# Kernel tuning notes

Hardware: AMD Instinct MI355X
Metric: run time of the kernel (lower is better)

## Reference

```python
import jax, jax.numpy as jnp
import numpy as np

D = 256
K = 3  # depthwise conv kernel size (odd)
A_EPS = 1e-4
POW_MIN = 1e-20
LN_EPS = 1e-5


def setup_inputs() -> dict:
    key = jax.random.key(0)
    ks = jax.random.split(key, 10)
    B, H, W = 8, 96, 96
    x = jax.random.normal(ks[0], (B, H, W, D), dtype=jnp.float32)
    inp = {
        'x': x,
        'ln_g': jnp.ones((D,), jnp.float32),
        'ln_b': jnp.zeros((D,), jnp.float32),
        'w_in': jax.random.normal(ks[1], (D, 2 * D), jnp.float32) * 0.02,
        'b_in': jnp.zeros((2 * D,), jnp.float32),
        'conv_w': jax.random.normal(ks[2], (K, K, 1, D), jnp.float32) * 0.1,
        'conv_b': jnp.zeros((D,), jnp.float32),
        'a_logit': 7.0 + 0.1 * jax.random.normal(ks[3], (D,), jnp.float32),
        'ssm_b': jnp.ones((D,), jnp.float32) + 0.02 * jax.random.normal(ks[4], (D,), jnp.float32),
        'ssm_c': jnp.ones((D,), jnp.float32) + 0.02 * jax.random.normal(ks[5], (D,), jnp.float32),
        'ssm_d': jnp.ones((D,), jnp.float32) + 0.02 * jax.random.normal(ks[6], (D,), jnp.float32),
        'w_out': jax.random.normal(ks[7], (D, D), jnp.float32) * 0.02,
        'b_out': jnp.zeros((D,), jnp.float32),
    }
    return inp


def _ssm_scan(x, a_logit, b, c, d):
    # x: (N, L, D). s_t = a*s_{t-1} + b*x_t ; y_t = c*s_t + d*x_t
    # via log-domain cumsum reformulation (as in the torch source).
    L = x.shape[1]
    a = jnp.clip(jax.nn.sigmoid(a_logit), A_EPS, 1.0 - A_EPS)  # (D,)
    t = jnp.arange(L, dtype=jnp.float32)
    a_pow = jnp.maximum(jnp.exp(t[:, None] * jnp.log(a)[None, :]), POW_MIN)  # (L,D)
    u = x * b  # (N,L,D)
    r = jnp.cumsum(u / a_pow[None], axis=1)
    return r * a_pow[None] * c + x * d


def reference(x, ln_g, ln_b, w_in, b_in, conv_w, conv_b,
              a_logit, ssm_b, ssm_c, ssm_d, w_out, b_out):
    B, H, W, Dm = x.shape
    x0 = x
    # LayerNorm over channel dim
    mu = jnp.mean(x, axis=-1, keepdims=True)
    var = jnp.mean(jnp.square(x - mu), axis=-1, keepdims=True)
    h = (x - mu) * jax.lax.rsqrt(var + LN_EPS) * ln_g + ln_b
    # in_proj -> split into value and gate
    xg = h @ w_in + b_in  # (B,H,W,2D)
    x_in, gate = jnp.split(xg, 2, axis=-1)
    gate = jax.nn.sigmoid(gate)
    # depthwise conv (SAME padding) + SiLU, NHWC layout
    u = jax.lax.conv_general_dilated(
        x_in, conv_w, window_strides=(1, 1), padding='SAME',
        dimension_numbers=('NHWC', 'HWIO', 'NHWC'), feature_group_count=Dm)
    u = jax.nn.silu(u + conv_b)
    # 2D bidirectional scan mixing
    L = H * W
    seq_row = u.reshape(B, L, Dm)
    seq_col = u.transpose(0, 2, 1, 3).reshape(B, L, Dm)

    def bid(s):
        yf = _ssm_scan(s, a_logit, ssm_b, ssm_c, ssm_d)
        yb = jnp.flip(_ssm_scan(jnp.flip(s, axis=1), a_logit, ssm_b, ssm_c, ssm_d), axis=1)
        return 0.5 * (yf + yb)

    y_row = bid(seq_row).reshape(B, H, W, Dm)
    y_col = bid(seq_col).reshape(B, W, H, Dm).transpose(0, 2, 1, 3)
    y = 0.5 * (y_row + y_col)
    # gate, out_proj, residual
    y = y * gate
    y = y @ w_out + b_out
    return x0 + y
```

## Files before the change

### kernel.cpp

```cpp
#include <hip/hip_runtime.h>
#include <math.h>

#define DD   256
#define HHH  96
#define WWW  96
#define NB   8
#define LL   9216
#define NPIX (NB*LL)
#define TCH  32
#define NCH  (LL/TCH)

typedef __bf16 bf16_8 __attribute__((ext_vector_type(8)));
typedef float  f32_4  __attribute__((ext_vector_type(4)));

static __device__ __forceinline__ float sigmoidf_(float x) {
    return 1.0f / (1.0f + expf(-x));
}

template<int DIR>
static __device__ __forceinline__ int spidx(int t) {
    if (DIR == 0) return t;
    int w = t / HHH;
    int h = t - w * HHH;
    return h * WWW + w;
}

__global__ __launch_bounds__(256) void wcvt_kernel(const float* __restrict__ w_in,
                                                   const float* __restrict__ w_out,
                                                   __bf16* __restrict__ w_inT,
                                                   __bf16* __restrict__ w_outT) {
    int i = blockIdx.x * 256 + threadIdx.x;
    int n = i >> 8, k = i & 255;
    w_inT[i] = (__bf16)w_in[k * 512 + n];
    if (i < 256 * 256) w_outT[i] = (__bf16)w_out[k * 256 + n];
}

__global__ __launch_bounds__(256) void ln_kernel(const float* __restrict__ x,
                                                 const float* __restrict__ g,
                                                 const float* __restrict__ b,
                                                 __bf16* __restrict__ h) {
    int pix = blockIdx.x;
    int d = threadIdx.x;
    float v = x[(size_t)pix * DD + d];
    float s = v, s2 = v * v;
    #pragma unroll
    for (int o = 32; o > 0; o >>= 1) {
        s  += __shfl_down(s, o, 64);
        s2 += __shfl_down(s2, o, 64);
    }
    __shared__ float ws1[4], ws2[4];
    int wid = d >> 6, lane = d & 63;
    if (lane == 0) { ws1[wid] = s; ws2[wid] = s2; }
    __syncthreads();
    if (d == 0) {
        float a = 0.f, c = 0.f;
        for (int i = 0; i < 4; i++) { a += ws1[i]; c += ws2[i]; }
        ws1[0] = a; ws2[0] = c;
    }
    __syncthreads();
    float mu  = ws1[0] * (1.0f / 256.0f);
    float var = ws2[0] * (1.0f / 256.0f) - mu * mu;
    float r = rsqrtf(var + 1e-5f);
    h[(size_t)pix * DD + d] = (__bf16)((v - mu) * r * g[d] + b[d]);
}

template<int MODE>
__global__ __launch_bounds__(256) void gemm_bf16(const __bf16* __restrict__ A,
                                                 const __bf16* __restrict__ BT,
                                                 const float* __restrict__ bias,
                                                 __bf16* __restrict__ out_xin,
                                                 __bf16* __restrict__ out_gate,
                                                 float* __restrict__ out_f32,
                                                 const float* __restrict__ x0) {
    const int K = 256;
    __shared__ __bf16 As[128 * 40];
    __shared__ __bf16 Bs[128 * 40];
    int tid = threadIdx.x;
    int lane = tid & 63, wv = tid >> 6;
    int rowBase = blockIdx.x * 128;
    int colBase = blockIdx.y * 128;
    int ldr = tid >> 2;
    int seg = tid & 3;

    f32_4 acc[4][4];
    #pragma unroll
    for (int i = 0; i < 4; i++)
        #pragma unroll
        for (int j = 0; j < 4; j++) acc[i][j] = (f32_4){0.f, 0.f, 0.f, 0.f};

    const __bf16* Aip = A + (size_t)(rowBase + ldr) * K + seg * 8;
    const __bf16* Bip = BT + (size_t)(colBase + ldr) * K + seg * 8;
    int m0 = (wv >> 1) * 64, n0 = (wv & 1) * 64;
    int fr = lane & 15, fq = lane >> 4;

    for (int k0 = 0; k0 < K; k0 += 32) {
        uint4 a0 = *(const uint4*)(Aip + k0);
        uint4 a1 = *(const uint4*)(Aip + (size_t)64 * K + k0);
        uint4 b0 = *(const uint4*)(Bip + k0);
        uint4 b1 = *(const uint4*)(Bip + (size_t)64 * K + k0);
        __syncthreads();
        *(uint4*)&As[ldr * 40 + seg * 8]        = a0;
        *(uint4*)&As[(ldr + 64) * 40 + seg * 8] = a1;
        *(uint4*)&Bs[ldr * 40 + seg * 8]        = b0;
        *(uint4*)&Bs[(ldr + 64) * 40 + seg * 8] = b1;
        __syncthreads();
        bf16_8 af[4], bb[4];
        #pragma unroll
        for (int mi = 0; mi < 4; mi++)
            af[mi] = *(const bf16_8*)&As[(m0 + mi * 16 + fr) * 40 + fq * 8];
        #pragma unroll
        for (int ni = 0; ni < 4; ni++)
            bb[ni] = *(const bf16_8*)&Bs[(n0 + ni * 16 + fr) * 40 + fq * 8];
        #pragma unroll
        for (int mi = 0; mi < 4; mi++)
            #pragma unroll
            for (int ni = 0; ni < 4; ni++)
                acc[mi][ni] = __builtin_amdgcn_mfma_f32_16x16x32_bf16(
                    af[mi], bb[ni], acc[mi][ni], 0, 0, 0);
    }

    int rowW = rowBase + m0 + fq * 4;
    int colW = colBase + n0 + fr;
    #pragma unroll
    for (int mi = 0; mi < 4; mi++) {
        #pragma unroll
        for (int ni = 0; ni < 4; ni++) {
            int col = colW + ni * 16;
            float bv = bias[col];
            #pragma unroll
            for (int r = 0; r < 4; r++) {
                int row = rowW + mi * 16 + r;
                float v = acc[mi][ni][r] + bv;
                if (MODE == 0) {
                    if (col < 256) {
                        out_xin[(size_t)row * 256 + col] = (__bf16)v;
                    } else {
                        out_gate[(size_t)row * 256 + (col - 256)] = (__bf16)sigmoidf_(v);
                    }
                } else {
                    out_f32[(size_t)row * 256 + col] = v + x0[(size_t)row * 256 + col];
                }
            }
        }
    }
}

static __device__ __forceinline__ void loadcol(const __bf16* __restrict__ xin,
                                               int b, int h, int w, int d,
                                               float c[3]) {
    if (w < 0 || w >= WWW) { c[0] = c[1] = c[2] = 0.f; return; }
    size_t base = ((size_t)b * LL + (size_t)h * WWW + w) * DD + d;
    c[0] = (h > 0)       ? (float)xin[base - (size_t)WWW * DD] : 0.f;
    c[1] = (float)xin[base];
    c[2] = (h + 1 < HHH) ? (float)xin[base + (size_t)WWW * DD] : 0.f;
}

__global__ __launch_bounds__(256) void conv_tot_kernel(const __bf16* __restrict__ xin,
                                                       const float* __restrict__ cw,
                                                       const float* __restrict__ cb,
                                                       const float* __restrict__ a_logit,
                                                       const float* __restrict__ ssm_b,
                                                       __bf16* __restrict__ u,
                                                       float* __restrict__ tot_f,
                                                       float* __restrict__ tot_b) {
    int cx = blockIdx.x, h = blockIdx.y, b = blockIdx.z;
    int d = threadIdx.x;
    int w0 = cx * TCH;
    float k[9];
    #pragma unroll
    for (int i = 0; i < 9; i++) k[i] = cw[i * DD + d];
    float bias = cb[d];
    float a = sigmoidf_(a_logit[d]);
    a = fminf(fmaxf(a, 1e-4f), 1.0f - 1e-4f);
    float bb = ssm_b[d];

    float cl[3], cc[3], cr[3];
    loadcol(xin, b, h, w0 - 1, d, cl);
    loadcol(xin, b, h, w0,     d, cc);
    loadcol(xin, b, h, w0 + 1, d, cr);

    float v[TCH];
    float sf = 0.f;
    size_t outBase = ((size_t)b * LL + (size_t)h * WWW + w0) * DD + d;
    #pragma unroll
    for (int j = 0; j < TCH; j++) {
        float nx[3];
        loadcol(xin, b, h, w0 + j + 2, d, nx);
        float acc = bias;
        acc += k[0] * cl[0] + k[1] * cc[0] + k[2] * cr[0];
        acc += k[3] * cl[1] + k[4] * cc[1] + k[5] * cr[1];
        acc += k[6] * cl[2] + k[7] * cc[2] + k[8] * cr[2];
        float uv = acc * sigmoidf_(acc);
        v[j] = uv;
        u[outBase + (size_t)j * DD] = (__bf16)uv;
        sf = a * sf + bb * uv;
        cl[0] = cc[0]; cl[1] = cc[1]; cl[2] = cc[2];
        cc[0] = cr[0]; cc[1] = cr[1]; cc[2] = cr[2];
        cr[0] = nx[0]; cr[1] = nx[1]; cr[2] = nx[2];
    }
    int chunk = h * 3 + cx;
    tot_f[((size_t)b * NCH + chunk) * DD + d] = sf;
    float sb = 0.f;
    #pragma unroll
    for (int j = TCH - 1; j >= 0; j--) sb = a * sb + bb * v[j];
    tot_b[((size_t)b * NCH + chunk) * DD + d] = sb;
}

__global__ __launch_bounds__(256) void scan_totals_col(const __bf16* __restrict__ u,
                                                       const float* __restrict__ a_logit,
                                                       const float* __restrict__ ssm_b,
                                                       float* __restrict__ tot_f,
                                                       float* __restrict__ tot_b) {
    int blk = blockIdx.x;
    int b = blk / NCH, c = blk - b * NCH;
    int d = threadIdx.x;
    float a = sigmoidf_(a_logit[d]);
    a = fminf(fmaxf(a, 1e-4f), 1.0f - 1e-4f);
    float bb = ssm_b[d];
    size_t base = (size_t)b * LL * DD;
    int t0 = c * TCH;
    float v[TCH];
    #pragma unroll
    for (int j = 0; j < TCH; j++)
        v[j] = (float)u[base + (size_t)spidx<1>(t0 + j) * DD + d];
    float s = 0.f;
    #pragma unroll
    for (int j = 0; j < TCH; j++) s = a * s + bb * v[j];
    tot_f[(size_t)blk * DD + d] = s;
    s = 0.f;
    #pragma unroll
    for (int j = TCH - 1; j >= 0; j--) s = a * s + bb * v[j];
    tot_b[(size_t)blk * DD + d] = s;
}

__global__ __launch_bounds__(256) void scan_carries(const float* __restrict__ tot_all,
                                                    const float* __restrict__ a_logit,
                                                    float* __restrict__ car_all) {
    int b = blockIdx.x;
    int var = blockIdx.y;
    int d = threadIdx.x;
    float a = sigmoidf_(a_logit[d]);
    a = fminf(fmaxf(a, 1e-4f), 1.0f - 1e-4f);
    float a2 = a * a, a4 = a2 * a2, a8 = a4 * a4, a16 = a8 * a8;
    float q = a16 * a16;
    const float* tot = tot_all + (size_t)var * NB * NCH * DD + (size_t)b * NCH * DD + d;
    float* car = car_all + (size_t)var * NB * NCH * DD + (size_t)b * NCH * DD + d;
    float P = 0.f;
    if ((var & 1) == 0) {
        for (int c0 = 0; c0 < NCH; c0 += 8) {
            float t[8];
            #pragma unroll
            for (int j = 0; j < 8; j++) t[j] = tot[(size_t)(c0 + j) * DD];
            #pragma unroll
            for (int j = 0; j < 8; j++) {
                car[(size_t)(c0 + j) * DD] = P;
                P = q * P + t[j];
            }
        }
    } else {
        for (int c0 = NCH - 8; c0 >= 0; c0 -= 8) {
            float t[8];
            #pragma unroll
            for (int j = 0; j < 8; j++) t[j] = tot[(size_t)(c0 + j) * DD];
            #pragma unroll
            for (int j = 7; j >= 0; j--) {
                car[(size_t)(c0 + j) * DD] = P;
                P = q * P + t[j];
            }
        }
    }
}

template<int DIR>
__global__ __launch_bounds__(256) void scan_apply(const __bf16* __restrict__ u,
                                                  const float* __restrict__ a_logit,
                                                  const float* __restrict__ ssm_b,
                                                  const float* __restrict__ ssm_c,
                                                  const float* __restrict__ ssm_d,
                                                  const float* __restrict__ car_f,
                                                  const float* __restrict__ car_b,
                                                  float* __restrict__ y,
                                                  const __bf16* __restrict__ gate,
                                                  __bf16* __restrict__ g) {
    int blk = blockIdx.x;
    int b = blk / NCH, c = blk - b * NCH;
    int d = threadIdx.x;
    float a = sigmoidf_(a_logit[d]);
    a = fminf(fmaxf(a, 1e-4f), 1.0f - 1e-4f);
    float bb = ssm_b[d], cc = ssm_c[d], dd = ssm_d[d];
    size_t base = (size_t)b * LL * DD;
    int t0 = c * TCH;
    float v[TCH];
    #pragma unroll
    for (int j = 0; j < TCH; j++)
        v[j] = (float)u[base + (size_t)spidx<DIR>(t0 + j) * DD + d];
    float yf[TCH];
    float s = car_f[(size_t)blk * DD + d];
    #pragma unroll
    for (int j = 0; j < TCH; j++) {
        s = a * s + bb * v[j];
        yf[j] = cc * s + dd * v[j];
    }
    s = car_b[(size_t)blk * DD + d];
    #pragma unroll
    for (int j = TCH - 1; j >= 0; j--) {
        s = a * s + bb * v[j];
        float val = 0.25f * (yf[j] + cc * s + dd * v[j]);
        size_t idx = base + (size_t)spidx<DIR>(t0 + j) * DD + d;
        if (DIR == 0) {
            y[idx] = val;
        } else {
            float t = y[idx] + val;
            g[idx] = (__bf16)(t * (float)gate[idx]);
        }
    }
}

extern "C" void kernel_launch(void* const* d_in, const int* in_sizes, int n_in,
                              void* d_out, int out_size, void* d_ws, size_t ws_size,
                              hipStream_t stream) {
    const float* x       = (const float*)d_in[0];
    const float* ln_g    = (const float*)d_in[1];
    const float* ln_b    = (const float*)d_in[2];
    const float* w_in    = (const float*)d_in[3];
    const float* b_in    = (const float*)d_in[4];
    const float* conv_w  = (const float*)d_in[5];
    const float* conv_b  = (const float*)d_in[6];
    const float* a_logit = (const float*)d_in[7];
    const float* ssm_b   = (const float*)d_in[8];
    const float* ssm_c   = (const float*)d_in[9];
    const float* ssm_d   = (const float*)d_in[10];
    const float* w_out   = (const float*)d_in[11];
    const float* b_out   = (const float*)d_in[12];
    float* out = (float*)d_out;

    char* ws = (char*)d_ws;
    const size_t SZH = (size_t)NPIX * DD * sizeof(__bf16);
    const size_t TS  = (size_t)NB * NCH * DD * sizeof(float);

    __bf16* hB     = (__bf16*)(ws);
    __bf16* xinB   = (__bf16*)(ws + SZH);
    __bf16* uB     = (__bf16*)(ws + 2 * SZH);
    __bf16* gateB  = (__bf16*)(ws + 3 * SZH);
    float*  tot    = (float*)(ws + 4 * SZH);
    float*  car    = (float*)(ws + 4 * SZH + 4 * TS);
    __bf16* w_inT  = (__bf16*)(ws + 4 * SZH + 8 * TS);
    __bf16* w_outT = w_inT + 512 * 256;
    float* y = out;

    wcvt_kernel<<<512, 256, 0, stream>>>(w_in, w_out, w_inT, w_outT);
    ln_kernel<<<NPIX, 256, 0, stream>>>(x, ln_g, ln_b, hB);
    gemm_bf16<0><<<dim3(NPIX / 128, 4), 256, 0, stream>>>(hB, w_inT, b_in,
                                                          xinB, gateB, nullptr, nullptr);
    conv_tot_kernel<<<dim3(WWW / TCH, HHH, NB), 256, 0, stream>>>(
        xinB, conv_w, conv_b, a_logit, ssm_b, uB,
        tot + 0 * (size_t)NB * NCH * DD, tot + 1 * (size_t)NB * NCH * DD);
    scan_totals_col<<<NB * NCH, 256, 0, stream>>>(
        uB, a_logit, ssm_b,
        tot + 2 * (size_t)NB * NCH * DD, tot + 3 * (size_t)NB * NCH * DD);
    scan_carries<<<dim3(NB, 4), 256, 0, stream>>>(tot, a_logit, car);
    scan_apply<0><<<NB * NCH, 256, 0, stream>>>(
        uB, a_logit, ssm_b, ssm_c, ssm_d,
        car + 0 * (size_t)NB * NCH * DD, car + 1 * (size_t)NB * NCH * DD,
        y, nullptr, nullptr);
    scan_apply<1><<<NB * NCH, 256, 0, stream>>>(
        uB, a_logit, ssm_b, ssm_c, ssm_d,
        car + 2 * (size_t)NB * NCH * DD, car + 3 * (size_t)NB * NCH * DD,
        y, gateB, hB);
    gemm_bf16<1><<<dim3(NPIX / 128, 2), 256, 0, stream>>>(hB, w_outT, b_out,
                                                          nullptr, nullptr, out, x);
}
```

Measured before the change: 451.4 us.

## Double-buffer GEMM tiles with direct global-to-LDS loads and vectorize LayerNorm

The bf16 MFMA GEMM now uses two LDS buffers filled by global_load_lds, so the next K-slice is fetched while the current one is computed. This drops the register round-trip and one of the two barriers per iteration. The unpadded BK=32 layout may cause LDS bank conflicts on fragment reads. LayerNorm now handles one pixel per wavefront with float4 loads and xor-shuffle reductions, which removes shared memory and block-wide syncs.

```diff
diff --git a/kernel.cpp b/kernel.cpp
--- a/kernel.cpp
+++ b/kernel.cpp
@@ -17,6 +17,12 @@
     return 1.0f / (1.0f + expf(-x));
 }
 
+typedef const __attribute__((address_space(1))) void gas_void;
+typedef __attribute__((address_space(3))) void las_void;
+static __device__ __forceinline__ void glld16(const void* g, void* l) {
+    __builtin_amdgcn_global_load_lds((gas_void*)g, (las_void*)l, 16, 0, 0);
+}
+
 template<int DIR>
 static __device__ __forceinline__ int spidx(int t) {
     if (DIR == 0) return t;
@@ -39,29 +45,27 @@
                                                  const float* __restrict__ g,
                                                  const float* __restrict__ b,
                                                  __bf16* __restrict__ h) {
-    int pix = blockIdx.x;
-    int d = threadIdx.x;
-    float v = x[(size_t)pix * DD + d];
-    float s = v, s2 = v * v;
+    int wv = threadIdx.x >> 6, lane = threadIdx.x & 63;
+    int pix = blockIdx.x * 4 + wv;
+    const float4 v = *(const float4*)&x[(size_t)pix * DD + lane * 4];
+    float s  = v.x + v.y + v.z + v.w;
+    float s2 = v.x * v.x + v.y * v.y + v.z * v.z + v.w * v.w;
     #pragma unroll
     for (int o = 32; o > 0; o >>= 1) {
-        s  += __shfl_down(s, o, 64);
-        s2 += __shfl_down(s2, o, 64);
-    }
-    __shared__ float ws1[4], ws2[4];
-    int wid = d >> 6, lane = d & 63;
-    if (lane == 0) { ws1[wid] = s; ws2[wid] = s2; }
-    __syncthreads();
-    if (d == 0) {
-        float a = 0.f, c = 0.f;
-        for (int i = 0; i < 4; i++) { a += ws1[i]; c += ws2[i]; }
-        ws1[0] = a; ws2[0] = c;
-    }
-    __syncthreads();
-    float mu  = ws1[0] * (1.0f / 256.0f);
-    float var = ws2[0] * (1.0f / 256.0f) - mu * mu;
+        s  += __shfl_xor(s, o, 64);
+        s2 += __shfl_xor(s2, o, 64);
+    }
+    float mu  = s * (1.0f / 256.0f);
+    float var = s2 * (1.0f / 256.0f) - mu * mu;
     float r = rsqrtf(var + 1e-5f);
-    h[(size_t)pix * DD + d] = (__bf16)((v - mu) * r * g[d] + b[d]);
+    float4 gg = *(const float4*)&g[lane * 4];
+    float4 bb = *(const float4*)&b[lane * 4];
+    union { ushort4 u; __bf16 e[4]; } o4;
+    o4.e[0] = (__bf16)((v.x - mu) * r * gg.x + bb.x);
+    o4.e[1] = (__bf16)((v.y - mu) * r * gg.y + bb.y);
+    o4.e[2] = (__bf16)((v.z - mu) * r * gg.z + bb.z);
+    o4.e[3] = (__bf16)((v.w - mu) * r * gg.w + bb.w);
+    *(ushort4*)&h[(size_t)pix * DD + lane * 4] = o4.u;
 }
 
 template<int MODE>
@@ -73,51 +77,60 @@
                                                  float* __restrict__ out_f32,
                                                  const float* __restrict__ x0) {
     const int K = 256;
-    __shared__ __bf16 As[128 * 40];
-    __shared__ __bf16 Bs[128 * 40];
+    const int BK = 32;
+    __shared__ __bf16 As[2][128 * BK];
+    __shared__ __bf16 Bs[2][128 * BK];
     int tid = threadIdx.x;
     int lane = tid & 63, wv = tid >> 6;
     int rowBase = blockIdx.x * 128;
     int colBase = blockIdx.y * 128;
-    int ldr = tid >> 2;
-    int seg = tid & 3;
-
-    f32_4 acc[4][4];
-    #pragma unroll
-    for (int i = 0; i < 4; i++)
-        #pragma unroll
-        for (int j = 0; j < 4; j++) acc[i][j] = (f32_4){0.f, 0.f, 0.f, 0.f};
-
-    const __bf16* Aip = A + (size_t)(rowBase + ldr) * K + seg * 8;
-    const __bf16* Bip = BT + (size_t)(colBase + ldr) * K + seg * 8;
+
+    int srow = tid >> 2, sseg = tid & 3;
+    const __bf16* aS0 = A  + (size_t)(rowBase + srow) * K + sseg * 8;
+    const __bf16* aS1 = A  + (size_t)(rowBase + srow + 64) * K + sseg * 8;
+    const __bf16* bS0 = BT + (size_t)(colBase + srow) * K + sseg * 8;
+    const __bf16* bS1 = BT + (size_t)(colBase + srow + 64) * K + sseg * 8;
+    int wvoff = wv * 1024;
+
     int m0 = (wv >> 1) * 64, n0 = (wv & 1) * 64;
     int fr = lane & 15, fq = lane >> 4;
 
-    for (int k0 = 0; k0 < K; k0 += 32) {
-        uint4 a0 = *(const uint4*)(Aip + k0);
-        uint4 a1 = *(const uint4*)(Aip + (size_t)64 * K + k0);
-        uint4 b0 = *(const uint4*)(Bip + k0);
-        uint4 b1 = *(const uint4*)(Bip + (size_t)64 * K + k0);
-        __syncthreads();
-        *(uint4*)&As[ldr * 40 + seg * 8]        = a0;
-        *(uint4*)&As[(ldr + 64) * 40 + seg * 8] = a1;
-        *(uint4*)&Bs[ldr * 40 + seg * 8]        = b0;
-        *(uint4*)&Bs[(ldr + 64) * 40 + seg * 8] = b1;
-        __syncthreads();
+    f32_4 acc[4][4];
+    #pragma unroll
+    for (int i = 0; i < 4; i++)
+        #pragma unroll
+        for (int j = 0; j < 4; j++) acc[i][j] = (f32_4){0.f, 0.f, 0.f, 0.f};
+
+#define STAGE(bufi, koff)                                                  \
+    do {                                                                   \
+        glld16(aS0 + (koff), (char*)&As[bufi][0] + wvoff);                 \
+        glld16(aS1 + (koff), (char*)&As[bufi][0] + 4096 + wvoff);          \
+        glld16(bS0 + (koff), (char*)&Bs[bufi][0] + wvoff);                 \
+        glld16(bS1 + (koff), (char*)&Bs[bufi][0] + 4096 + wvoff);          \
+    } while (0)
+
+    STAGE(0, 0);
+    __syncthreads();
+    int cur = 0;
+    for (int t = 0; t < 8; ++t) {
+        if (t < 7) STAGE(cur ^ 1, (t + 1) * BK);
         bf16_8 af[4], bb[4];
         #pragma unroll
         for (int mi = 0; mi < 4; mi++)
-            af[mi] = *(const bf16_8*)&As[(m0 + mi * 16 + fr) * 40 + fq * 8];
+            af[mi] = *(const bf16_8*)&As[cur][(m0 + mi * 16 + fr) * BK + fq * 8];
         #pragma unroll
         for (int ni = 0; ni < 4; ni++)
-            bb[ni] = *(const bf16_8*)&Bs[(n0 + ni * 16 + fr) * 40 + fq * 8];
+            bb[ni] = *(const bf16_8*)&Bs[cur][(n0 + ni * 16 + fr) * BK + fq * 8];
         #pragma unroll
         for (int mi = 0; mi < 4; mi++)
             #pragma unroll
             for (int ni = 0; ni < 4; ni++)
                 acc[mi][ni] = __builtin_amdgcn_mfma_f32_16x16x32_bf16(
                     af[mi], bb[ni], acc[mi][ni], 0, 0, 0);
-    }
+        __syncthreads();
+        cur ^= 1;
+    }
+#undef STAGE
 
     int rowW = rowBase + m0 + fq * 4;
     int colW = colBase + n0 + fr;
@@ -349,7 +362,7 @@
     float* y = out;
 
     wcvt_kernel<<<512, 256, 0, stream>>>(w_in, w_out, w_inT, w_outT);
-    ln_kernel<<<NPIX, 256, 0, stream>>>(x, ln_g, ln_b, hB);
+    ln_kernel<<<NPIX / 4, 256, 0, stream>>>(x, ln_g, ln_b, hB);
     gemm_bf16<0><<<dim3(NPIX / 128, 4), 256, 0, stream>>>(hB, w_inT, b_in,
                                                           xinB, gateB, nullptr, nullptr);
     conv_tot_kernel<<<dim3(WWW / TCH, HHH, NB), 256, 0, stream>>>(
```

Result: faster. 410.8 us (-9.0%).
